# Kernel optimization log

Measured on AMD Instinct MI355X. Metric: run time of the kernel, lower is better.

Reference implementation:

```python
import jax, jax.numpy as jnp
import numpy as np

NUM_CLASSES = 19  # number of distinct labels in targets (fill_max)


def setup_inputs() -> dict:
    key = jax.random.key(0)
    k1, k2 = jax.random.split(key)
    n, d = 262144, 128
    inputs = jax.random.normal(k1, (n, d), dtype=jnp.float32)
    targets = jax.random.randint(k2, (n,), 0, NUM_CLASSES, dtype=jnp.int64)
    return {"inputs": inputs, "targets": targets}


def reference(inputs, targets):
    # Same math as the O(n^2) torch loop: for each sample i, the center is the
    # mean of all samples sharing targets[i]. Computed as one segment-reduction
    # over labels followed by a gather.
    n = inputs.shape[0]
    sums = jax.ops.segment_sum(inputs, targets, num_segments=NUM_CLASSES)          # [C, d]
    counts = jax.ops.segment_sum(jnp.ones((n,), inputs.dtype), targets,
                                 num_segments=NUM_CLASSES)                          # [C]
    class_centers = sums / counts[:, None]                                          # [C, d]
    centers = class_centers[targets]                                                # [n, d]
    dist_pc = jnp.sqrt(jnp.sum((inputs - centers) ** 2, axis=1))                    # [n]
    return jnp.mean(dist_pc)
```

## Files before the change

### kernel.cpp

```cpp
#include <hip/hip_runtime.h>
#include <math.h>

#define NCLS 19
#define DIM  128
#define CD   (NCLS * DIM)
#define GPB  8

__global__ __launch_bounds__(256) void k_accum(const float4* __restrict__ in4,
                                               const int* __restrict__ tgt,
                                               float* __restrict__ gsums,
                                               int* __restrict__ gcounts,
                                               int n) {
    __shared__ __align__(16) float ls[GPB * CD];
    __shared__ int lcnt[GPB * NCLS];
    const int tid = threadIdx.x;
    const int g   = tid >> 5;
    const int l32 = tid & 31;
    float* tbl = &ls[g * CD];
    int*   cnt = &lcnt[g * NCLS];

    for (int i = tid; i < GPB * CD; i += 256) ls[i] = 0.0f;
    for (int i = tid; i < GPB * NCLS; i += 256) lcnt[i] = 0;
    __syncthreads();

    const int stride = gridDim.x * GPB;
    int row = blockIdx.x * GPB + g;

    for (; row + 3 * stride < n; row += 4 * stride) {
        float4 v0 = in4[(size_t)(row             ) * 32 + l32];
        float4 v1 = in4[(size_t)(row +     stride) * 32 + l32];
        float4 v2 = in4[(size_t)(row + 2 * stride) * 32 + l32];
        float4 v3 = in4[(size_t)(row + 3 * stride) * 32 + l32];
        int c0 = tgt[row];
        int c1 = tgt[row + stride];
        int c2 = tgt[row + 2 * stride];
        int c3 = tgt[row + 3 * stride];
        float4* p;
        float4 a;
        p = (float4*)&tbl[c0 * DIM + l32 * 4];
        a = *p; a.x += v0.x; a.y += v0.y; a.z += v0.z; a.w += v0.w; *p = a;
        p = (float4*)&tbl[c1 * DIM + l32 * 4];
        a = *p; a.x += v1.x; a.y += v1.y; a.z += v1.z; a.w += v1.w; *p = a;
        p = (float4*)&tbl[c2 * DIM + l32 * 4];
        a = *p; a.x += v2.x; a.y += v2.y; a.z += v2.z; a.w += v2.w; *p = a;
        p = (float4*)&tbl[c3 * DIM + l32 * 4];
        a = *p; a.x += v3.x; a.y += v3.y; a.z += v3.z; a.w += v3.w; *p = a;
        if (l32 == 0) { cnt[c0]++; cnt[c1]++; cnt[c2]++; cnt[c3]++; }
    }
    for (; row < n; row += stride) {
        float4 v = in4[(size_t)row * 32 + l32];
        int c = tgt[row];
        float4* p = (float4*)&tbl[c * DIM + l32 * 4];
        float4 a = *p;
        a.x += v.x; a.y += v.y; a.z += v.z; a.w += v.w;
        *p = a;
        if (l32 == 0) cnt[c]++;
    }
    __syncthreads();

    for (int i = tid; i < CD; i += 256) {
        float s = 0.0f;
        #pragma unroll
        for (int gg = 0; gg < GPB; gg++) s += ls[gg * CD + i];
        unsafeAtomicAdd(&gsums[i], s);
    }
    if (tid < NCLS) {
        int s = 0;
        #pragma unroll
        for (int gg = 0; gg < GPB; gg++) s += lcnt[gg * NCLS + tid];
        atomicAdd(&gcounts[tid], s);
    }
}

__global__ __launch_bounds__(256) void k_dist(const float4* __restrict__ in4,
                                              const int* __restrict__ tgt,
                                              const float* __restrict__ gsums,
                                              const int* __restrict__ gcounts,
                                              float* __restrict__ out,
                                              int n, float inv_n) {
    __shared__ __align__(16) float lcent[CD];
    __shared__ float red[256];
    const int tid = threadIdx.x;

    for (int i = tid; i < CD; i += 256)
        lcent[i] = gsums[i] / (float)gcounts[i >> 7];
    __syncthreads();

    const int l32 = tid & 31;
    const int g   = tid >> 5;
    const int stride = gridDim.x * 8;
    float acc = 0.0f;
    int row = blockIdx.x * 8 + g;

    for (; row + 3 * stride < n; row += 4 * stride) {
        float4 v0 = in4[(size_t)(row             ) * 32 + l32];
        float4 v1 = in4[(size_t)(row +     stride) * 32 + l32];
        float4 v2 = in4[(size_t)(row + 2 * stride) * 32 + l32];
        float4 v3 = in4[(size_t)(row + 3 * stride) * 32 + l32];
        int c0 = tgt[row];
        int c1 = tgt[row + stride];
        int c2 = tgt[row + 2 * stride];
        int c3 = tgt[row + 3 * stride];
        float4 e0 = *(const float4*)&lcent[c0 * DIM + l32 * 4];
        float4 e1 = *(const float4*)&lcent[c1 * DIM + l32 * 4];
        float4 e2 = *(const float4*)&lcent[c2 * DIM + l32 * 4];
        float4 e3 = *(const float4*)&lcent[c3 * DIM + l32 * 4];
        float dx, dy, dz, dw;
        dx = v0.x - e0.x; dy = v0.y - e0.y; dz = v0.z - e0.z; dw = v0.w - e0.w;
        float d0 = dx * dx + dy * dy + dz * dz + dw * dw;
        dx = v1.x - e1.x; dy = v1.y - e1.y; dz = v1.z - e1.z; dw = v1.w - e1.w;
        float d1 = dx * dx + dy * dy + dz * dz + dw * dw;
        dx = v2.x - e2.x; dy = v2.y - e2.y; dz = v2.z - e2.z; dw = v2.w - e2.w;
        float d2 = dx * dx + dy * dy + dz * dz + dw * dw;
        dx = v3.x - e3.x; dy = v3.y - e3.y; dz = v3.z - e3.z; dw = v3.w - e3.w;
        float d3 = dx * dx + dy * dy + dz * dz + dw * dw;
        for (int off = 16; off > 0; off >>= 1) {
            d0 += __shfl_down(d0, off, 32);
            d1 += __shfl_down(d1, off, 32);
            d2 += __shfl_down(d2, off, 32);
            d3 += __shfl_down(d3, off, 32);
        }
        if (l32 == 0) acc += sqrtf(d0) + sqrtf(d1) + sqrtf(d2) + sqrtf(d3);
    }
    for (; row < n; row += stride) {
        float4 v = in4[(size_t)row * 32 + l32];
        int c = tgt[row];
        float4 ce = *(const float4*)&lcent[c * DIM + l32 * 4];
        float dx = v.x - ce.x, dy = v.y - ce.y, dz = v.z - ce.z, dw = v.w - ce.w;
        float d2 = dx * dx + dy * dy + dz * dz + dw * dw;
        for (int off = 16; off > 0; off >>= 1)
            d2 += __shfl_down(d2, off, 32);
        if (l32 == 0) acc += sqrtf(d2);
    }

    red[tid] = acc;
    __syncthreads();
    for (int s = 128; s > 0; s >>= 1) {
        if (tid < s) red[tid] += red[tid + s];
        __syncthreads();
    }
    if (tid == 0) unsafeAtomicAdd(out, red[0] * inv_n);
}

extern "C" void kernel_launch(void* const* d_in, const int* in_sizes, int n_in,
                              void* d_out, int out_size, void* d_ws, size_t ws_size,
                              hipStream_t stream) {
    const float* in  = (const float*)d_in[0];
    const int*   tgt = (const int*)d_in[1];
    const int n = in_sizes[0] / DIM;

    float* gsums   = (float*)d_ws;
    int*   gcounts = (int*)(gsums + CD);
    float* out     = (float*)d_out;

    hipMemsetAsync(d_ws, 0, CD * sizeof(float) + NCLS * sizeof(int), stream);
    hipMemsetAsync(d_out, 0, sizeof(float), stream);

    k_accum<<<512, 256, 0, stream>>>((const float4*)in, tgt, gsums, gcounts, n);
    k_dist<<<1024, 256, 0, stream>>>((const float4*)in, tgt, gsums, gcounts, out,
                                     n, 1.0f / (float)n);
}
```

Before: 234.1 us.

## Fuse accumulate and distance kernels with a software grid barrier

Merges the class-sum accumulation kernel and the distance kernel into one persistent kernel. An atomic counter in the workspace acts as a grid-wide barrier between the two phases, and the first phase's shared-memory table is reused to hold the class centers. The goal is to drop a kernel launch and the inter-kernel gap, and to have each block re-read the same rows it just accumulated so those reads are more likely to hit in cache. In exchange, correctness depends on all 512 blocks being resident at once; if they are not, the spin barrier deadlocks.

```diff
diff --git a/kernel.cpp b/kernel.cpp
--- a/kernel.cpp
+++ b/kernel.cpp
@@ -5,12 +5,15 @@
 #define DIM  128
 #define CD   (NCLS * DIM)
 #define GPB  8
+#define GRID 512
 
-__global__ __launch_bounds__(256) void k_accum(const float4* __restrict__ in4,
+__global__ __launch_bounds__(256) void k_fused(const float4* __restrict__ in4,
                                                const int* __restrict__ tgt,
                                                float* __restrict__ gsums,
                                                int* __restrict__ gcounts,
-                                               int n) {
+                                               int* __restrict__ bar,
+                                               float* __restrict__ out,
+                                               int n, float inv_n) {
     __shared__ __align__(16) float ls[GPB * CD];
     __shared__ int lcnt[GPB * NCLS];
     const int tid = threadIdx.x;
@@ -24,8 +27,9 @@
     __syncthreads();
 
     const int stride = gridDim.x * GPB;
-    int row = blockIdx.x * GPB + g;
+    const int row0 = blockIdx.x * GPB + g;
 
+    int row = row0;
     for (; row + 3 * stride < n; row += 4 * stride) {
         float4 v0 = in4[(size_t)(row             ) * 32 + l32];
         float4 v1 = in4[(size_t)(row +     stride) * 32 + l32];
@@ -70,28 +74,27 @@
         for (int gg = 0; gg < GPB; gg++) s += lcnt[gg * NCLS + tid];
         atomicAdd(&gcounts[tid], s);
     }
-}
-
-__global__ __launch_bounds__(256) void k_dist(const float4* __restrict__ in4,
-                                              const int* __restrict__ tgt,
-                                              const float* __restrict__ gsums,
-                                              const int* __restrict__ gcounts,
-                                              float* __restrict__ out,
-                                              int n, float inv_n) {
-    __shared__ __align__(16) float lcent[CD];
-    __shared__ float red[256];
-    const int tid = threadIdx.x;
-
-    for (int i = tid; i < CD; i += 256)
-        lcent[i] = gsums[i] / (float)gcounts[i >> 7];
     __syncthreads();
 
-    const int l32 = tid & 31;
-    const int g   = tid >> 5;
-    const int stride = gridDim.x * 8;
+    if (tid == 0) {
+        __hip_atomic_fetch_add(bar, 1, __ATOMIC_ACQ_REL, __HIP_MEMORY_SCOPE_AGENT);
+        while (__hip_atomic_load(bar, __ATOMIC_ACQUIRE, __HIP_MEMORY_SCOPE_AGENT)
+               < (int)gridDim.x)
+            __builtin_amdgcn_s_sleep(8);
+    }
+    __syncthreads();
+
+    for (int i = tid; i < CD; i += 256) {
+        float s = __hip_atomic_load(&gsums[i], __ATOMIC_RELAXED,
+                                    __HIP_MEMORY_SCOPE_AGENT);
+        int c = __hip_atomic_load(&gcounts[i >> 7], __ATOMIC_RELAXED,
+                                  __HIP_MEMORY_SCOPE_AGENT);
+        ls[i] = s / (float)c;
+    }
+    __syncthreads();
+
     float acc = 0.0f;
-    int row = blockIdx.x * 8 + g;
-
+    row = row0;
     for (; row + 3 * stride < n; row += 4 * stride) {
         float4 v0 = in4[(size_t)(row             ) * 32 + l32];
         float4 v1 = in4[(size_t)(row +     stride) * 32 + l32];
@@ -101,10 +104,10 @@
         int c1 = tgt[row + stride];
         int c2 = tgt[row + 2 * stride];
         int c3 = tgt[row + 3 * stride];
-        float4 e0 = *(const float4*)&lcent[c0 * DIM + l32 * 4];
-        float4 e1 = *(const float4*)&lcent[c1 * DIM + l32 * 4];
-        float4 e2 = *(const float4*)&lcent[c2 * DIM + l32 * 4];
-        float4 e3 = *(const float4*)&lcent[c3 * DIM + l32 * 4];
+        float4 e0 = *(const float4*)&ls[c0 * DIM + l32 * 4];
+        float4 e1 = *(const float4*)&ls[c1 * DIM + l32 * 4];
+        float4 e2 = *(const float4*)&ls[c2 * DIM + l32 * 4];
+        float4 e3 = *(const float4*)&ls[c3 * DIM + l32 * 4];
         float dx, dy, dz, dw;
         dx = v0.x - e0.x; dy = v0.y - e0.y; dz = v0.z - e0.z; dw = v0.w - e0.w;
         float d0 = dx * dx + dy * dy + dz * dz + dw * dw;
@@ -125,7 +128,7 @@
     for (; row < n; row += stride) {
         float4 v = in4[(size_t)row * 32 + l32];
         int c = tgt[row];
-        float4 ce = *(const float4*)&lcent[c * DIM + l32 * 4];
+        float4 ce = *(const float4*)&ls[c * DIM + l32 * 4];
         float dx = v.x - ce.x, dy = v.y - ce.y, dz = v.z - ce.z, dw = v.w - ce.w;
         float d2 = dx * dx + dy * dy + dz * dz + dw * dw;
         for (int off = 16; off > 0; off >>= 1)
@@ -133,6 +136,7 @@
         if (l32 == 0) acc += sqrtf(d2);
     }
 
+    float* red = &ls[CD];
     red[tid] = acc;
     __syncthreads();
     for (int s = 128; s > 0; s >>= 1) {
@@ -151,12 +155,12 @@
 
     float* gsums   = (float*)d_ws;
     int*   gcounts = (int*)(gsums + CD);
+    int*   bar     = gcounts + NCLS;
     float* out     = (float*)d_out;
 
-    hipMemsetAsync(d_ws, 0, CD * sizeof(float) + NCLS * sizeof(int), stream);
+    hipMemsetAsync(d_ws, 0, (CD + NCLS + 1) * sizeof(int), stream);
     hipMemsetAsync(d_out, 0, sizeof(float), stream);
 
-    k_accum<<<512, 256, 0, stream>>>((const float4*)in, tgt, gsums, gcounts, n);
-    k_dist<<<1024, 256, 0, stream>>>((const float4*)in, tgt, gsums, gcounts, out,
-                                     n, 1.0f / (float)n);
+    k_fused<<<GRID, 256, 0, stream>>>((const float4*)in, tgt, gsums, gcounts,
+                                      bar, out, n, 1.0f / (float)n);
 }
```

Result: slower. 268.5 us (+14.7%).
